# Kernel tuning notes

Measured on AMD Instinct MI355X. Metric: run time of the kernel, lower is better.

Reference implementation:

```python
import jax, jax.numpy as jnp
import numpy as np

N_HEADS = 16


def setup_inputs() -> dict:
    key = jax.random.key(0)
    ks = jax.random.split(key, 9)
    B, S, D = 2, 2048, 1024
    s = 0.02
    return {
        "x": jax.random.normal(ks[0], (B, S, D), dtype=jnp.float32),
        "Wq": jax.random.normal(ks[1], (D, D), dtype=jnp.float32) * s,
        "bq": jax.random.normal(ks[2], (D,), dtype=jnp.float32) * s,
        "Wk": jax.random.normal(ks[3], (D, D), dtype=jnp.float32) * s,
        "bk": jax.random.normal(ks[4], (D,), dtype=jnp.float32) * s,
        "Wv": jax.random.normal(ks[5], (D, D), dtype=jnp.float32) * s,
        "bv": jax.random.normal(ks[6], (D,), dtype=jnp.float32) * s,
        "Wo": jax.random.normal(ks[7], (D, D), dtype=jnp.float32) * s,
        "bo": jax.random.normal(ks[8], (D,), dtype=jnp.float32) * s,
    }


def reference(x, Wq, bq, Wk, bk, Wv, bv, Wo, bo):
    B, S, D = x.shape
    H = N_HEADS
    hd = D // H
    # projections -> [B, H, S, hd]
    def heads(w, b):
        return (x @ w + b).reshape(B, S, H, hd).transpose(0, 2, 1, 3)
    Q, K, V = heads(Wq, bq), heads(Wk, bk), heads(Wv, bv)
    scores = jnp.einsum("bhqd,bhkd->bhqk", Q, K)
    causal = jnp.triu(jnp.ones((S, S), dtype=bool), k=1)  # True above diagonal
    scores = jnp.where(causal, -jnp.inf, scores)
    w = jax.nn.softmax(scores / jnp.sqrt(jnp.float32(hd)), axis=-1)
    ctx = jnp.einsum("bhqk,bhkd->bhqd", w, V).transpose(0, 2, 1, 3).reshape(B, S, D)
    return ctx @ Wo + bo
```

## Files before the change

### kernel.cpp

```cpp
#include <hip/hip_runtime.h>
#include <hip/hip_bf16.h>

typedef __attribute__((ext_vector_type(8))) short short8;
typedef __attribute__((ext_vector_type(4))) float floatx4;

#define D_MODEL 1024
#define SEQ     2048
#define NB      2
#define NH      16
#define HD      64
#define MROWS   4096
#define CZ      (0.125f * 1.44269504f)

__device__ __forceinline__ floatx4 mfma_bf16(short8 a, short8 b, floatx4 c) {
  return __builtin_amdgcn_mfma_f32_16x16x32_bf16(a, b, c, 0, 0, 0);
}

__device__ __forceinline__ void dma16(const __hip_bfloat16* g, __hip_bfloat16* l) {
  __builtin_amdgcn_global_load_lds(
      (const __attribute__((address_space(1))) void*)g,
      (__attribute__((address_space(3))) void*)l, 16, 0, 0);
}
#define WAIT_VM0()  __asm__ __volatile__("s_waitcnt vmcnt(0)" ::: "memory")
#define WAIT_LGKM() __asm__ __volatile__("s_waitcnt lgkmcnt(0)" ::: "memory")

__global__ void convert_x_kernel(const float* __restrict__ x, __hip_bfloat16* __restrict__ xb) {
  int i = (blockIdx.x * 256 + threadIdx.x) * 4;
  float4 v = *(const float4*)(x + i);
  __hip_bfloat16 tmp[4];
  tmp[0] = __float2bfloat16(v.x);
  tmp[1] = __float2bfloat16(v.y);
  tmp[2] = __float2bfloat16(v.z);
  tmp[3] = __float2bfloat16(v.w);
  *(ushort4*)(xb + i) = *(ushort4*)tmp;
}

__global__ void transpose_w_kernel(const float* __restrict__ W0, const float* __restrict__ W1,
                                   const float* __restrict__ W2, const float* __restrict__ W3,
                                   __hip_bfloat16* __restrict__ T0, __hip_bfloat16* __restrict__ T1,
                                   __hip_bfloat16* __restrict__ T2, __hip_bfloat16* __restrict__ T3) {
  const int z = blockIdx.z;
  const float* W = (z == 0) ? W0 : (z == 1) ? W1 : (z == 2) ? W2 : W3;
  __hip_bfloat16* Wt = (z == 0) ? T0 : (z == 1) ? T1 : (z == 2) ? T2 : T3;
  __shared__ float tile[32][33];
  int k0 = blockIdx.x * 32, n0 = blockIdx.y * 32;
  int tx = threadIdx.x, ty = threadIdx.y;
#pragma unroll
  for (int i = 0; i < 4; i++)
    tile[ty + 8 * i][tx] = W[(size_t)(k0 + ty + 8 * i) * D_MODEL + n0 + tx];
  __syncthreads();
#pragma unroll
  for (int i = 0; i < 4; i++)
    Wt[(size_t)(n0 + ty + 8 * i) * D_MODEL + k0 + tx] = __float2bfloat16(tile[tx][ty + 8 * i]);
}

template <int MODE>
__global__ __launch_bounds__(256) void gemm_kernel(
    const __hip_bfloat16* __restrict__ X,
    const __hip_bfloat16* __restrict__ Wt0, const __hip_bfloat16* __restrict__ Wt1,
    const __hip_bfloat16* __restrict__ Wt2,
    const float* __restrict__ b0, const float* __restrict__ b1, const float* __restrict__ b2,
    void* __restrict__ out0, void* __restrict__ out1, void* __restrict__ out2) {
  const int z = blockIdx.z;
  const __hip_bfloat16* Wt = (z == 0) ? Wt0 : (z == 1) ? Wt1 : Wt2;
  const float* bias = (z == 0) ? b0 : (z == 1) ? b1 : b2;
  void* outp = (z == 0) ? out0 : (z == 1) ? out1 : out2;
  const float scale = (MODE == 0 && z == 0) ? CZ : 1.f;

  __shared__ __attribute__((aligned(16))) __hip_bfloat16 As[2][128 * 32];
  __shared__ __attribute__((aligned(16))) __hip_bfloat16 Bs[2][128 * 32];

  const int m0 = blockIdx.x * 128;
  const int n0 = blockIdx.y * 128;
  const int t = threadIdx.x;
  const int lane = t & 63, w = t >> 6;
  const int wm = (w >> 1) * 64, wn = (w & 1) * 64;
  const int lr = lane & 15;
  const int lq = lane >> 4;

  const __hip_bfloat16* Xp = X + (size_t)m0 * D_MODEL;
  const __hip_bfloat16* Wp = Wt + (size_t)n0 * D_MODEL;

  const int srow = (w << 5) + (lane >> 2);
  const int skg = (lane & 3) << 3;
  const int sbase0 = ((w << 5) << 5);
  const int sbase1 = (((w << 5) + 16) << 5);

  floatx4 acc[4][4];
#pragma unroll
  for (int i = 0; i < 4; i++)
#pragma unroll
    for (int j = 0; j < 4; j++) acc[i][j] = (floatx4){0.f, 0.f, 0.f, 0.f};

  dma16(Xp + (size_t)srow * D_MODEL + skg, &As[0][sbase0]);
  dma16(Xp + (size_t)(srow + 16) * D_MODEL + skg, &As[0][sbase1]);
  dma16(Wp + (size_t)srow * D_MODEL + skg, &Bs[0][sbase0]);
  dma16(Wp + (size_t)(srow + 16) * D_MODEL + skg, &Bs[0][sbase1]);

  for (int kt = 0; kt < 32; kt++) {
    WAIT_VM0();
    __syncthreads();
    if (kt + 1 < 32) {
      const int kn = (kt + 1) * 32;
      const int nb = (kt + 1) & 1;
      dma16(Xp + (size_t)srow * D_MODEL + kn + skg, &As[nb][sbase0]);
      dma16(Xp + (size_t)(srow + 16) * D_MODEL + kn + skg, &As[nb][sbase1]);
      dma16(Wp + (size_t)srow * D_MODEL + kn + skg, &Bs[nb][sbase0]);
      dma16(Wp + (size_t)(srow + 16) * D_MODEL + kn + skg, &Bs[nb][sbase1]);
    }
    const __hip_bfloat16* Ac = As[kt & 1];
    const __hip_bfloat16* Bc = Bs[kt & 1];
    short8 af[4], bfr[4];
#pragma unroll
    for (int i = 0; i < 4; i++) af[i] = *(const short8*)&Ac[(wm + i * 16 + lr) * 32 + lq * 8];
#pragma unroll
    for (int j = 0; j < 4; j++) bfr[j] = *(const short8*)&Bc[(wn + j * 16 + lr) * 32 + lq * 8];
#pragma unroll
    for (int i = 0; i < 4; i++)
#pragma unroll
      for (int j = 0; j < 4; j++) acc[i][j] = mfma_bf16(af[i], bfr[j], acc[i][j]);
  }

#pragma unroll
  for (int j = 0; j < 4; j++) {
    const int n = n0 + wn + j * 16 + lr;
    const float bv = bias[n];
#pragma unroll
    for (int i = 0; i < 4; i++) {
      const int mb = m0 + wm + i * 16 + lq * 4;
      if (MODE == 0) {
        __hip_bfloat16* O = (__hip_bfloat16*)outp;
        const int b = mb >> 11, s = mb & 2047;
        const int h = n >> 6, d = n & 63;
        if (z == 2) {
          ushort4 pk;
          __hip_bfloat16* pp = (__hip_bfloat16*)&pk;
#pragma unroll
          for (int r = 0; r < 4; r++) pp[r] = __float2bfloat16(acc[i][j][r] + bv);
          *(ushort4*)(O + (((size_t)(b * NH + h) * HD + d) * SEQ + s)) = pk;
        } else {
#pragma unroll
          for (int r = 0; r < 4; r++)
            O[(((size_t)(b * NH + h) * SEQ + (s + r)) * HD) + d] =
                __float2bfloat16((acc[i][j][r] + bv) * scale);
        }
      } else {
#pragma unroll
        for (int r = 0; r < 4; r++)
          ((float*)outp)[(size_t)(mb + r) * D_MODEL + n] = acc[i][j][r] + bv;
      }
    }
  }
}

__global__ __launch_bounds__(256, 2) void attn_kernel(
    const __hip_bfloat16* __restrict__ Q, const __hip_bfloat16* __restrict__ Kg,
    const __hip_bfloat16* __restrict__ Vt, __hip_bfloat16* __restrict__ ctx) {
  const int bh = blockIdx.y;
  const int b = bh >> 4, h = bh & 15;
  const int p = blockIdx.x;
  const int t = threadIdx.x, lane = t & 63, w = t >> 6;
  const int lr = lane & 15, lq = lane >> 4;

  __shared__ __attribute__((aligned(16))) __hip_bfloat16 Ks[2][64 * 64];
  __shared__ __attribute__((aligned(16))) __hip_bfloat16 VTs[2][64 * 64];
  __shared__ __attribute__((aligned(16))) __hip_bfloat16 Ps[4][16 * 72];

  const __hip_bfloat16* Qb = Q + (size_t)bh * SEQ * HD;
  const __hip_bfloat16* Kb = Kg + (size_t)bh * SEQ * HD;
  const __hip_bfloat16* Vb = Vt + (size_t)bh * HD * SEQ;

  const int srow0 = (w << 4) + (lane >> 3);
  const int sgl = lane & 7;
  const int sb0 = ((w << 4) << 6);
  const int sb1 = (((w << 4) + 8) << 6);

  const int nkt0 = p + 1;
  const int TOT = 33;

#define STAGE(nn, nb)                                                                  \
  {                                                                                    \
    const int r0 = srow0, r1 = srow0 + 8;                                              \
    dma16(Kb + ((size_t)((nn) + r0) << 6) + ((sgl ^ (r0 & 7)) << 3), &Ks[nb][sb0]);    \
    dma16(Kb + ((size_t)((nn) + r1) << 6) + ((sgl ^ (r1 & 7)) << 3), &Ks[nb][sb1]);    \
    dma16(Vb + (size_t)r0 * SEQ + (nn) + ((sgl ^ (r0 & 7)) << 3), &VTs[nb][sb0]);      \
    dma16(Vb + (size_t)r1 * SEQ + (nn) + ((sgl ^ (r1 & 7)) << 3), &VTs[nb][sb1]);      \
  }

  STAGE(0, 0);
  int g = 0;

  for (int ph = 0; ph < 2; ph++) {
    const int qt = ph ? 31 - p : p;
    const int nkt = qt + 1;
    const int rw = qt * 64 + w * 16;

    short8 qf[2];
#pragma unroll
    for (int ks = 0; ks < 2; ks++)
      qf[ks] = *(const short8*)(Qb + (size_t)(rw + lr) * HD + ks * 32 + lq * 8);

    floatx4 o[4];
#pragma unroll
    for (int dt = 0; dt < 4; dt++) o[dt] = (floatx4){0.f, 0.f, 0.f, 0.f};
    float ls[4] = {0.f, 0.f, 0.f, 0.f};

    for (int kt = 0; kt < nkt; kt++, g++) {
      WAIT_VM0();
      __syncthreads();
      const int gn = g + 1;
      if (gn < TOT) {
        const int ktn = (gn < nkt0) ? gn : gn - nkt0;
        const int nb = gn & 1;
        STAGE(ktn * 64, nb);
      }
      const __hip_bfloat16* Kc = Ks[g & 1];
      const __hip_bfloat16* Vc = VTs[g & 1];
      __hip_bfloat16* PsW = Ps[w];

      floatx4 s[4];
#pragma unroll
      for (int nt = 0; nt < 4; nt++) s[nt] = (floatx4){0.f, 0.f, 0.f, 0.f};
#pragma unroll
      for (int ks = 0; ks < 2; ks++) {
#pragma unroll
        for (int nt = 0; nt < 4; nt++) {
          const int key = nt * 16 + lr;
          short8 kf = *(const short8*)&Kc[(key << 6) + (((ks * 4 + lq) ^ (key & 7)) << 3)];
          s[nt] = mfma_bf16(qf[ks], kf, s[nt]);
        }
      }

      const int n0 = kt * 64;
      if (kt == nkt - 1) {
#pragma unroll
        for (int nt = 0; nt < 4; nt++)
#pragma unroll
          for (int r = 0; r < 4; r++) {
            const int row = rw + lq * 4 + r;
            const int key = n0 + nt * 16 + lr;
            float pe = (key <= row) ? exp2f(s[nt][r]) : 0.f;
            ls[r] += pe;
            PsW[(lq * 4 + r) * 72 + nt * 16 + lr] = __float2bfloat16(pe);
          }
      } else {
#pragma unroll
        for (int nt = 0; nt < 4; nt++)
#pragma unroll
          for (int r = 0; r < 4; r++) {
            float pe = exp2f(s[nt][r]);
            ls[r] += pe;
            PsW[(lq * 4 + r) * 72 + nt * 16 + lr] = __float2bfloat16(pe);
          }
      }
      WAIT_LGKM();

#pragma unroll
      for (int ks = 0; ks < 2; ks++) {
        short8 pf = *(const short8*)&PsW[lr * 72 + ks * 32 + lq * 8];
#pragma unroll
        for (int dt = 0; dt < 4; dt++) {
          const int d = dt * 16 + lr;
          short8 vf = *(const short8*)&Vc[(d << 6) + (((ks * 4 + lq) ^ (d & 7)) << 3)];
          o[dt] = mfma_bf16(pf, vf, o[dt]);
        }
      }
    }

    float inv[4];
#pragma unroll
    for (int r = 0; r < 4; r++) {
      float v = ls[r];
#pragma unroll
      for (int m = 8; m >= 1; m >>= 1) v += __shfl_xor(v, m, 16);
      inv[r] = 1.f / v;
    }
    __hip_bfloat16* cp = ctx + (size_t)b * SEQ * D_MODEL + h * HD;
#pragma unroll
    for (int dt = 0; dt < 4; dt++)
#pragma unroll
      for (int r = 0; r < 4; r++) {
        const int s = rw + lq * 4 + r;
        cp[(size_t)s * D_MODEL + dt * 16 + lr] = __float2bfloat16(o[dt][r] * inv[r]);
      }
  }
#undef STAGE
}

extern "C" void kernel_launch(void* const* d_in, const int* in_sizes, int n_in,
                              void* d_out, int out_size, void* d_ws, size_t ws_size,
                              hipStream_t stream) {
  const float* x  = (const float*)d_in[0];
  const float* Wq = (const float*)d_in[1];
  const float* bq = (const float*)d_in[2];
  const float* Wk = (const float*)d_in[3];
  const float* bk = (const float*)d_in[4];
  const float* Wv = (const float*)d_in[5];
  const float* bv = (const float*)d_in[6];
  const float* Wo = (const float*)d_in[7];
  const float* bo = (const float*)d_in[8];

  char* ws = (char*)d_ws;
  const size_t MB = 1u << 20;
  __hip_bfloat16* xb  = (__hip_bfloat16*)(ws + 0 * MB);
  __hip_bfloat16* wtq = (__hip_bfloat16*)(ws + 8 * MB);
  __hip_bfloat16* wtk = (__hip_bfloat16*)(ws + 10 * MB);
  __hip_bfloat16* wtv = (__hip_bfloat16*)(ws + 12 * MB);
  __hip_bfloat16* wto = (__hip_bfloat16*)(ws + 14 * MB);
  __hip_bfloat16* qb  = (__hip_bfloat16*)(ws + 16 * MB);
  __hip_bfloat16* kb  = (__hip_bfloat16*)(ws + 24 * MB);
  __hip_bfloat16* vt  = (__hip_bfloat16*)(ws + 32 * MB);
  __hip_bfloat16* ctx = xb;

  convert_x_kernel<<<4096, 256, 0, stream>>>(x, xb);
  transpose_w_kernel<<<dim3(32, 32, 4), dim3(32, 8), 0, stream>>>(Wq, Wk, Wv, Wo,
                                                                  wtq, wtk, wtv, wto);
  gemm_kernel<0><<<dim3(32, 8, 3), 256, 0, stream>>>(xb, wtq, wtk, wtv, bq, bk, bv,
                                                     (void*)qb, (void*)kb, (void*)vt);
  attn_kernel<<<dim3(16, 32), 256, 0, stream>>>(qb, kb, vt, ctx);
  gemm_kernel<1><<<dim3(32, 8, 1), 256, 0, stream>>>(ctx, wto, wto, wto, bo, bo, bo,
                                                     d_out, d_out, d_out);
}
```

Before: 203.6 us.

## Triple-buffer GEMM and attention loads with partial vmcnt waits, reorder grids

Both the GEMM and attention kernels move from double to triple buffering in LDS, staging two tiles ahead and waiting only on the older loads (partial vmcnt) before a raw s_barrier. The goal is to hide global-to-LDS latency. The output GEMM uses a 64-row M tile so it launches more blocks, and grid dimensions are reordered so blocks that share weights or K/V run close together. Attention also preloads Q fragments for both phases up front. Costs are more LDS per block, which may cut occupancy, and hand-counted vmcnt values that must match the number of DMA issues per stage.

```diff
diff --git a/kernel.cpp b/kernel.cpp
--- a/kernel.cpp
+++ b/kernel.cpp
@@ -21,7 +21,8 @@
       (const __attribute__((address_space(1))) void*)g,
       (__attribute__((address_space(3))) void*)l, 16, 0, 0);
 }
-#define WAIT_VM0()  __asm__ __volatile__("s_waitcnt vmcnt(0)" ::: "memory")
+#define WAIT_VM(n)  __asm__ __volatile__("s_waitcnt vmcnt(" #n ")" ::: "memory")
+#define BARRIER()   __asm__ __volatile__("s_barrier" ::: "memory")
 #define WAIT_LGKM() __asm__ __volatile__("s_waitcnt lgkmcnt(0)" ::: "memory")
 
 __global__ void convert_x_kernel(const float* __restrict__ x, __hip_bfloat16* __restrict__ xb) {
@@ -61,72 +62,91 @@
     const __hip_bfloat16* __restrict__ Wt2,
     const float* __restrict__ b0, const float* __restrict__ b1, const float* __restrict__ b2,
     void* __restrict__ out0, void* __restrict__ out1, void* __restrict__ out2) {
-  const int z = blockIdx.z;
+  constexpr int MT = (MODE == 0) ? 128 : 64;
+  constexpr int I = MT / 32;
+  constexpr int NKT = D_MODEL / 32;
+
+  const int z = blockIdx.y;
   const __hip_bfloat16* Wt = (z == 0) ? Wt0 : (z == 1) ? Wt1 : Wt2;
   const float* bias = (z == 0) ? b0 : (z == 1) ? b1 : b2;
   void* outp = (z == 0) ? out0 : (z == 1) ? out1 : out2;
   const float scale = (MODE == 0 && z == 0) ? CZ : 1.f;
 
-  __shared__ __attribute__((aligned(16))) __hip_bfloat16 As[2][128 * 32];
-  __shared__ __attribute__((aligned(16))) __hip_bfloat16 Bs[2][128 * 32];
-
-  const int m0 = blockIdx.x * 128;
-  const int n0 = blockIdx.y * 128;
+  __shared__ __attribute__((aligned(16))) __hip_bfloat16 As[3][MT * 32];
+  __shared__ __attribute__((aligned(16))) __hip_bfloat16 Bs[3][128 * 32];
+
+  const int n0 = blockIdx.x * 128;
+  const int m0 = blockIdx.z * MT;
   const int t = threadIdx.x;
   const int lane = t & 63, w = t >> 6;
-  const int wm = (w >> 1) * 64, wn = (w & 1) * 64;
+  const int wm = (w >> 1) * (MT / 2), wn = (w & 1) * 64;
   const int lr = lane & 15;
   const int lq = lane >> 4;
 
   const __hip_bfloat16* Xp = X + (size_t)m0 * D_MODEL;
   const __hip_bfloat16* Wp = Wt + (size_t)n0 * D_MODEL;
 
-  const int srow = (w << 5) + (lane >> 2);
+  const int lrow = lane >> 2;
   const int skg = (lane & 3) << 3;
-  const int sbase0 = ((w << 5) << 5);
-  const int sbase1 = (((w << 5) + 16) << 5);
-
-  floatx4 acc[4][4];
-#pragma unroll
-  for (int i = 0; i < 4; i++)
+  const int srowA = ((MT == 128) ? (w << 5) : (w << 4)) + lrow;
+  const int sbA0 = (((MT == 128) ? (w << 5) : (w << 4)) << 5);
+  const int sbA1 = sbA0 + (16 << 5);
+  const int srowB = (w << 5) + lrow;
+  const int sbB0 = ((w << 5) << 5);
+  const int sbB1 = sbB0 + (16 << 5);
+
+#define STAGE_G(kt_, buf_)                                                              \
+  {                                                                                     \
+    const int kn_ = (kt_) * 32;                                                         \
+    dma16(Xp + (size_t)srowA * D_MODEL + kn_ + skg, &As[buf_][sbA0]);                   \
+    if (MT == 128) dma16(Xp + (size_t)(srowA + 16) * D_MODEL + kn_ + skg, &As[buf_][sbA1]); \
+    dma16(Wp + (size_t)srowB * D_MODEL + kn_ + skg, &Bs[buf_][sbB0]);                   \
+    dma16(Wp + (size_t)(srowB + 16) * D_MODEL + kn_ + skg, &Bs[buf_][sbB1]);            \
+  }
+
+  floatx4 acc[I][4];
+#pragma unroll
+  for (int i = 0; i < I; i++)
 #pragma unroll
     for (int j = 0; j < 4; j++) acc[i][j] = (floatx4){0.f, 0.f, 0.f, 0.f};
 
-  dma16(Xp + (size_t)srow * D_MODEL + skg, &As[0][sbase0]);
-  dma16(Xp + (size_t)(srow + 16) * D_MODEL + skg, &As[0][sbase1]);
-  dma16(Wp + (size_t)srow * D_MODEL + skg, &Bs[0][sbase0]);
-  dma16(Wp + (size_t)(srow + 16) * D_MODEL + skg, &Bs[0][sbase1]);
-
-  for (int kt = 0; kt < 32; kt++) {
-    WAIT_VM0();
-    __syncthreads();
-    if (kt + 1 < 32) {
-      const int kn = (kt + 1) * 32;
-      const int nb = (kt + 1) & 1;
-      dma16(Xp + (size_t)srow * D_MODEL + kn + skg, &As[nb][sbase0]);
-      dma16(Xp + (size_t)(srow + 16) * D_MODEL + kn + skg, &As[nb][sbase1]);
-      dma16(Wp + (size_t)srow * D_MODEL + kn + skg, &Bs[nb][sbase0]);
-      dma16(Wp + (size_t)(srow + 16) * D_MODEL + kn + skg, &Bs[nb][sbase1]);
-    }
-    const __hip_bfloat16* Ac = As[kt & 1];
-    const __hip_bfloat16* Bc = Bs[kt & 1];
-    short8 af[4], bfr[4];
-#pragma unroll
-    for (int i = 0; i < 4; i++) af[i] = *(const short8*)&Ac[(wm + i * 16 + lr) * 32 + lq * 8];
+  STAGE_G(0, 0);
+  STAGE_G(1, 1);
+
+  int cb = 0;
+  for (int kt = 0; kt < NKT; kt++) {
+    if (kt < NKT - 1) {
+      if constexpr (MODE == 0) WAIT_VM(4);
+      else                     WAIT_VM(3);
+    } else {
+      WAIT_VM(0);
+    }
+    BARRIER();
+    if (kt + 2 < NKT) {
+      const int nb = (cb == 0) ? 2 : cb - 1;
+      STAGE_G(kt + 2, nb);
+    }
+    const __hip_bfloat16* Ac = As[cb];
+    const __hip_bfloat16* Bc = Bs[cb];
+    short8 af[I], bfr[4];
+#pragma unroll
+    for (int i = 0; i < I; i++) af[i] = *(const short8*)&Ac[(wm + i * 16 + lr) * 32 + lq * 8];
 #pragma unroll
     for (int j = 0; j < 4; j++) bfr[j] = *(const short8*)&Bc[(wn + j * 16 + lr) * 32 + lq * 8];
 #pragma unroll
-    for (int i = 0; i < 4; i++)
+    for (int i = 0; i < I; i++)
 #pragma unroll
       for (int j = 0; j < 4; j++) acc[i][j] = mfma_bf16(af[i], bfr[j], acc[i][j]);
-  }
+    cb = (cb == 2) ? 0 : cb + 1;
+  }
+#undef STAGE_G
 
 #pragma unroll
   for (int j = 0; j < 4; j++) {
     const int n = n0 + wn + j * 16 + lr;
     const float bv = bias[n];
 #pragma unroll
-    for (int i = 0; i < 4; i++) {
+    for (int i = 0; i < I; i++) {
       const int mb = m0 + wm + i * 16 + lq * 4;
       if (MODE == 0) {
         __hip_bfloat16* O = (__hip_bfloat16*)outp;
@@ -156,19 +176,29 @@
 __global__ __launch_bounds__(256, 2) void attn_kernel(
     const __hip_bfloat16* __restrict__ Q, const __hip_bfloat16* __restrict__ Kg,
     const __hip_bfloat16* __restrict__ Vt, __hip_bfloat16* __restrict__ ctx) {
-  const int bh = blockIdx.y;
+  const int bh = blockIdx.x;
   const int b = bh >> 4, h = bh & 15;
-  const int p = blockIdx.x;
+  const int p = blockIdx.y;
   const int t = threadIdx.x, lane = t & 63, w = t >> 6;
   const int lr = lane & 15, lq = lane >> 4;
 
-  __shared__ __attribute__((aligned(16))) __hip_bfloat16 Ks[2][64 * 64];
-  __shared__ __attribute__((aligned(16))) __hip_bfloat16 VTs[2][64 * 64];
+  __shared__ __attribute__((aligned(16))) __hip_bfloat16 Ks[3][64 * 64];
+  __shared__ __attribute__((aligned(16))) __hip_bfloat16 VTs[3][64 * 64];
   __shared__ __attribute__((aligned(16))) __hip_bfloat16 Ps[4][16 * 72];
 
   const __hip_bfloat16* Qb = Q + (size_t)bh * SEQ * HD;
   const __hip_bfloat16* Kb = Kg + (size_t)bh * SEQ * HD;
   const __hip_bfloat16* Vb = Vt + (size_t)bh * HD * SEQ;
+
+  short8 qf[2][2];
+#pragma unroll
+  for (int ph = 0; ph < 2; ph++) {
+    const int qt = ph ? 31 - p : p;
+    const int rw = qt * 64 + w * 16;
+#pragma unroll
+    for (int ks = 0; ks < 2; ks++)
+      qf[ph][ks] = *(const short8*)(Qb + (size_t)(rw + lr) * HD + ks * 32 + lq * 8);
+  }
 
   const int srow0 = (w << 4) + (lane >> 3);
   const int sgl = lane & 7;
@@ -186,36 +216,33 @@
     dma16(Vb + (size_t)r0 * SEQ + (nn) + ((sgl ^ (r0 & 7)) << 3), &VTs[nb][sb0]);      \
     dma16(Vb + (size_t)r1 * SEQ + (nn) + ((sgl ^ (r1 & 7)) << 3), &VTs[nb][sb1]);      \
   }
-
-  STAGE(0, 0);
-  int g = 0;
+#define KTN(gs) (((gs) < nkt0) ? (gs) : (gs)-nkt0)
+
+  STAGE(KTN(0) * 64, 0);
+  STAGE(KTN(1) * 64, 1);
+  int g = 0, cb = 0;
 
   for (int ph = 0; ph < 2; ph++) {
     const int qt = ph ? 31 - p : p;
     const int nkt = qt + 1;
     const int rw = qt * 64 + w * 16;
 
-    short8 qf[2];
-#pragma unroll
-    for (int ks = 0; ks < 2; ks++)
-      qf[ks] = *(const short8*)(Qb + (size_t)(rw + lr) * HD + ks * 32 + lq * 8);
-
     floatx4 o[4];
 #pragma unroll
     for (int dt = 0; dt < 4; dt++) o[dt] = (floatx4){0.f, 0.f, 0.f, 0.f};
     float ls[4] = {0.f, 0.f, 0.f, 0.f};
 
     for (int kt = 0; kt < nkt; kt++, g++) {
-      WAIT_VM0();
-      __syncthreads();
-      const int gn = g + 1;
-      if (gn < TOT) {
-        const int ktn = (gn < nkt0) ? gn : gn - nkt0;
-        const int nb = gn & 1;
-        STAGE(ktn * 64, nb);
-      }
-      const __hip_bfloat16* Kc = Ks[g & 1];
-      const __hip_bfloat16* Vc = VTs[g & 1];
+      if (g < TOT - 1) WAIT_VM(4);
+      else             WAIT_VM(0);
+      BARRIER();
+      if (g + 2 < TOT) {
+        const int nb = (cb == 0) ? 2 : cb - 1;
+        STAGE(KTN(g + 2) * 64, nb);
+      }
+      const __hip_bfloat16* Kc = Ks[cb];
+      const __hip_bfloat16* Vc = VTs[cb];
+      cb = (cb == 2) ? 0 : cb + 1;
       __hip_bfloat16* PsW = Ps[w];
 
       floatx4 s[4];
@@ -227,7 +254,7 @@
         for (int nt = 0; nt < 4; nt++) {
           const int key = nt * 16 + lr;
           short8 kf = *(const short8*)&Kc[(key << 6) + (((ks * 4 + lq) ^ (key & 7)) << 3)];
-          s[nt] = mfma_bf16(qf[ks], kf, s[nt]);
+          s[nt] = mfma_bf16(qf[ph][ks], kf, s[nt]);
         }
       }
 
@@ -285,6 +312,7 @@
       }
   }
 #undef STAGE
+#undef KTN
 }
 
 extern "C" void kernel_launch(void* const* d_in, const int* in_sizes, int n_in,
@@ -315,9 +343,9 @@
   convert_x_kernel<<<4096, 256, 0, stream>>>(x, xb);
   transpose_w_kernel<<<dim3(32, 32, 4), dim3(32, 8), 0, stream>>>(Wq, Wk, Wv, Wo,
                                                                   wtq, wtk, wtv, wto);
-  gemm_kernel<0><<<dim3(32, 8, 3), 256, 0, stream>>>(xb, wtq, wtk, wtv, bq, bk, bv,
+  gemm_kernel<0><<<dim3(8, 3, 32), 256, 0, stream>>>(xb, wtq, wtk, wtv, bq, bk, bv,
                                                      (void*)qb, (void*)kb, (void*)vt);
-  attn_kernel<<<dim3(16, 32), 256, 0, stream>>>(qb, kb, vt, ctx);
-  gemm_kernel<1><<<dim3(32, 8, 1), 256, 0, stream>>>(ctx, wto, wto, wto, bo, bo, bo,
+  attn_kernel<<<dim3(32, 16), 256, 0, stream>>>(qb, kb, vt, ctx);
+  gemm_kernel<1><<<dim3(8, 1, 64), 256, 0, stream>>>(ctx, wto, wto, wto, bo, bo, bo,
                                                      d_out, d_out, d_out);
 }
```

Result: faster. 198.4 us (-2.5%).
